# Performance work log

Hardware: AMD Instinct MI355X
Metric: run time of the kernel (lower is better)

## Reference

```python
import jax, jax.numpy as jnp
import numpy as np

D_MODEL = 1024
N_HEADS = 16
HEAD_DIM = D_MODEL // N_HEADS


def setup_inputs() -> dict:
    key = jax.random.key(0)
    ks = jax.random.split(key, 5)
    T, B = 2048, 2
    x = jax.random.normal(ks[0], (T, B, D_MODEL), dtype=jnp.float32)
    s = 1.0 / np.sqrt(D_MODEL)
    Wq = jax.random.normal(ks[1], (D_MODEL, D_MODEL), dtype=jnp.float32) * s
    Wk = jax.random.normal(ks[2], (D_MODEL, D_MODEL), dtype=jnp.float32) * s
    Wv = jax.random.normal(ks[3], (D_MODEL, D_MODEL), dtype=jnp.float32) * s
    Wo = jax.random.normal(ks[4], (D_MODEL, D_MODEL), dtype=jnp.float32) * s
    return {"x": x, "Wq": Wq, "Wk": Wk, "Wv": Wv, "Wo": Wo}


def reference(x, Wq, Wk, Wv, Wo):
    T, B, C = x.shape
    H, D = N_HEADS, HEAD_DIM

    def split_heads(t):
        # (T,B,C) -> (B,H,T,D), matching view+permute(1,2,0,3)
        return t.reshape(T, B, H, D).transpose(1, 2, 0, 3)

    q = split_heads(x @ Wq.T)
    k = split_heads(x @ Wk.T)
    v = split_heads(x @ Wv.T)

    scale = 1.0 / jnp.sqrt(jnp.asarray(D, dtype=x.dtype))
    scores = jnp.einsum('bhqd,bhkd->bhqk', q, k) * scale  # (B,H,T,T)
    causal = jnp.tril(jnp.ones((T, T), dtype=bool))
    scores = jnp.where(causal, scores, jnp.asarray(-jnp.inf, dtype=scores.dtype))
    probs = jax.nn.softmax(scores, axis=-1)
    ctx = jnp.einsum('bhqk,bhkd->bhqd', probs, v)  # (B,H,T,D)
    ctx = ctx.transpose(2, 0, 1, 3).reshape(T, B, C)
    return ctx @ Wo.T
```

## Files before the change

kernel.cpp:

```cpp
#include <hip/hip_runtime.h>
#include <hip/hip_bf16.h>

#define TT 2048
#define BB 2
#define CC 1024
#define HH 16
#define DD 64
#define MM (TT * BB)

typedef short bf16x8 __attribute__((ext_vector_type(8)));
typedef float f32x4  __attribute__((ext_vector_type(4)));

__device__ inline ushort f2b(float f) {
    union { float f; unsigned u; } v; v.f = f;
    unsigned r = v.u + 0x7FFFu + ((v.u >> 16) & 1u);
    return (ushort)(r >> 16);
}

__device__ inline unsigned pack_bf16(float a, float b) {
    __hip_bfloat162 h = __float22bfloat162_rn(make_float2(a, b));
    union { __hip_bfloat162 h; unsigned u; } c; c.h = h;
    return c.u;
}

__device__ inline void gload_lds16(const ushort* g, ushort* l) {
    __builtin_amdgcn_global_load_lds(
        (const __attribute__((address_space(1))) void*)g,
        (__attribute__((address_space(3))) void*)l, 16, 0, 0);
}

__global__ __launch_bounds__(256) void conv_x(const float* __restrict__ src,
                                              ushort* __restrict__ dst) {
    int i = blockIdx.x * 256 + threadIdx.x;
    float4 v = ((const float4*)src)[i];
    ushort4 o = {f2b(v.x), f2b(v.y), f2b(v.z), f2b(v.w)};
    ((ushort4*)dst)[i] = o;
}

__global__ __launch_bounds__(256) void conv_w(const float* __restrict__ Wq,
                                              const float* __restrict__ Wk,
                                              const float* __restrict__ Wv,
                                              const float* __restrict__ Wo,
                                              ushort* __restrict__ dst) {
    const float* s = (blockIdx.y == 0) ? Wq : (blockIdx.y == 1) ? Wk
                   : (blockIdx.y == 2) ? Wv : Wo;
    int i = blockIdx.x * 256 + threadIdx.x;
    float4 v = ((const float4*)s)[i];
    ushort4 o = {f2b(v.x), f2b(v.y), f2b(v.z), f2b(v.w)};
    ((ushort4*)(dst + (size_t)blockIdx.y * CC * CC))[i] = o;
}

template <int MODE>
__global__ __launch_bounds__(256) void gemm_mfma(const ushort* __restrict__ A,
                                                 const ushort* __restrict__ B0,
                                                 const ushort* __restrict__ B1,
                                                 const ushort* __restrict__ B2,
                                                 ushort* __restrict__ Oq,
                                                 ushort* __restrict__ Ok,
                                                 ushort* __restrict__ Ov,
                                                 float* __restrict__ Of) {
    __shared__ __align__(16) ushort As[128 * 32];
    __shared__ __align__(16) ushort Bs[128 * 32];

    const int tid = threadIdx.x;
    const int wave = tid >> 6, lane = tid & 63;
    const int quad = lane >> 4, l16 = lane & 15;
    const int wm = wave >> 1, wn = wave & 1;

    const int bm = blockIdx.x * 128;
    const ushort* Bp;
    int bn, wsel = 0;
    if (MODE == 1) {
        int by = blockIdx.y;
        wsel = by >> 3;
        Bp = (wsel == 0) ? B0 : (wsel == 1) ? B1 : B2;
        bn = (by & 7) * 128;
    } else {
        Bp = B0;
        bn = blockIdx.y * 128;
    }

    const int srow = lane >> 2;
    const int scol = (lane & 3) * 8;

    f32x4 acc[4][4];
#pragma unroll
    for (int i = 0; i < 4; i++)
#pragma unroll
        for (int j = 0; j < 4; j++) acc[i][j] = (f32x4){0.f, 0.f, 0.f, 0.f};

    for (int k0 = 0; k0 < CC; k0 += 32) {
#pragma unroll
        for (int i = 0; i < 2; i++) {
            const int rbase = wave * 32 + i * 16;
            gload_lds16(A + (size_t)(bm + rbase + srow) * CC + k0 + scol,
                        As + rbase * 32);
            gload_lds16(Bp + (size_t)(bn + rbase + srow) * CC + k0 + scol,
                        Bs + rbase * 32);
        }
        __syncthreads();

        bf16x8 af[4], bf[4];
#pragma unroll
        for (int mi = 0; mi < 4; mi++)
            af[mi] = *(const bf16x8*)(As + (wm * 64 + mi * 16 + l16) * 32 + quad * 8);
#pragma unroll
        for (int ni = 0; ni < 4; ni++)
            bf[ni] = *(const bf16x8*)(Bs + (wn * 64 + ni * 16 + l16) * 32 + quad * 8);
#pragma unroll
        for (int mi = 0; mi < 4; mi++)
#pragma unroll
            for (int ni = 0; ni < 4; ni++)
                acc[mi][ni] = __builtin_amdgcn_mfma_f32_16x16x32_bf16(
                    af[mi], bf[ni], acc[mi][ni], 0, 0, 0);
        __syncthreads();
    }

#pragma unroll
    for (int mi = 0; mi < 4; mi++) {
#pragma unroll
        for (int r = 0; r < 4; r++) {
            const int m = bm + wm * 64 + mi * 16 + quad * 4 + r;
#pragma unroll
            for (int ni = 0; ni < 4; ni++) {
                const int colg = bn + wn * 64 + ni * 16 + l16;
                float v = acc[mi][ni][r];
                if (MODE == 0) {
                    Of[(size_t)m * CC + colg] = v;
                } else {
                    if (wsel == 0) v *= 0.18033688f;
                    const int t = m >> 1, b = m & 1;
                    const int h = colg >> 6, d = colg & 63;
                    ushort* dst = (wsel == 0) ? Oq : (wsel == 1) ? Ok : Ov;
                    dst[(((size_t)(b * HH + h)) * TT + t) * DD + d] = f2b(v);
                }
            }
        }
    }
}

__global__ __launch_bounds__(256) void vtrans(const ushort* __restrict__ Vb,
                                              ushort* __restrict__ Vt) {
    __shared__ __align__(16) ushort Ls[64 * 80];
    const int bh = blockIdx.y;
    const int t0 = blockIdx.x * 64;
    const int e = threadIdx.x;
    const size_t bsrc = (size_t)bh * TT * DD;
    const size_t bdst = (size_t)bh * DD * TT;

#pragma unroll
    for (int p = 0; p < 2; p++) {
        int r = p * 32 + (e >> 3);
        int oct = e & 7;
        *(uint4*)(Ls + r * 80 + oct * 8) =
            *(const uint4*)(Vb + bsrc + (size_t)(t0 + r) * DD + oct * 8);
    }
    __syncthreads();
#pragma unroll
    for (int p = 0; p < 2; p++) {
        int d = p * 32 + (e >> 3);
        int toct = e & 7;
        ushort tmp[8];
#pragma unroll
        for (int u = 0; u < 8; u++) {
            int jp = toct * 8 + u;
            int js = (jp & 3) * 16 + (jp >> 2);
            tmp[u] = Ls[js * 80 + d];
        }
        *(uint4*)(Vt + bdst + (size_t)d * TT + t0 + toct * 8) = *(uint4*)tmp;
    }
}

template <bool DIAG>
__device__ __forceinline__ void attn_step(const bf16x8* qa, f32x4* Oacc,
                                          float* lrun,
                                          const bf16x8* kf, const bf16x8* vf,
                                          ushort* Pw, int j0, int qbase,
                                          int quad, int l16) {
    f32x4 S[4];
#pragma unroll
    for (int nb = 0; nb < 4; nb++) S[nb] = (f32x4){0.f, 0.f, 0.f, 0.f};
#pragma unroll
    for (int c = 0; c < 2; c++)
#pragma unroll
        for (int nb = 0; nb < 4; nb++)
            S[nb] = __builtin_amdgcn_mfma_f32_16x16x32_bf16(qa[c], kf[c * 4 + nb],
                                                            S[nb], 0, 0, 0);

#pragma unroll
    for (int r = 0; r < 4; r++) {
        const int qg = qbase + quad * 4 + r;
        float p[4];
#pragma unroll
        for (int nb = 0; nb < 4; nb++) {
            float s = S[nb][r];
            if (DIAG) {
                if (j0 + nb * 16 + l16 > qg) s = -1e30f;
            }
            p[nb] = __builtin_amdgcn_exp2f(fminf(s, 60.f));
        }
        lrun[r] += (p[0] + p[1]) + (p[2] + p[3]);
        uint2 w;
        w.x = pack_bf16(p[0], p[1]);
        w.y = pack_bf16(p[2], p[3]);
        *(uint2*)(Pw + (quad * 4 + r) * 72 + l16 * 4) = w;
    }

#pragma unroll
    for (int c = 0; c < 2; c++) {
        bf16x8 pa = *(const bf16x8*)(Pw + l16 * 72 + c * 32 + quad * 8);
#pragma unroll
        for (int db = 0; db < 4; db++)
            Oacc[db] = __builtin_amdgcn_mfma_f32_16x16x32_bf16(pa, vf[c * 4 + db],
                                                               Oacc[db], 0, 0, 0);
    }
}

__global__ __launch_bounds__(256, 2) void attn_mfma(const ushort* __restrict__ Qb,
                                                    const ushort* __restrict__ Kb,
                                                    const ushort* __restrict__ Vt,
                                                    ushort* __restrict__ ctx) {
    __shared__ __align__(16) ushort Ks[64 * 72];
    __shared__ __align__(16) ushort Vs[64 * 72];
    __shared__ __align__(16) ushort Ps[4 * 16 * 72];

    const int tid  = threadIdx.x;
    const int wave = tid >> 6;
    const int lane = tid & 63;
    const int quad = lane >> 4;
    const int l16  = lane & 15;

    const int p  = blockIdx.x;
    const int bh = blockIdx.y;
    const int qtA = p, qtB = (TT / 64 - 1) - p;
    const int q0A = qtA * 64 + wave * 16;
    const int q0B = qtB * 64 + wave * 16;

    const size_t baseQK = (size_t)bh * TT * DD;
    const size_t baseVt = (size_t)bh * DD * TT;

    bf16x8 qaA[2], qaB[2];
    {
        const ushort* qp = Qb + baseQK + (size_t)(q0A + l16) * DD + quad * 8;
        qaA[0] = *(const bf16x8*)(qp);
        qaA[1] = *(const bf16x8*)(qp + 32);
        const ushort* qp2 = Qb + baseQK + (size_t)(q0B + l16) * DD + quad * 8;
        qaB[0] = *(const bf16x8*)(qp2);
        qaB[1] = *(const bf16x8*)(qp2 + 32);
    }

    f32x4 OA[4], OB[4];
#pragma unroll
    for (int i = 0; i < 4; i++) {
        OA[i] = (f32x4){0.f, 0.f, 0.f, 0.f};
        OB[i] = (f32x4){0.f, 0.f, 0.f, 0.f};
    }
    float lA[4] = {0.f, 0.f, 0.f, 0.f};
    float lB[4] = {0.f, 0.f, 0.f, 0.f};

    ushort* Pw = Ps + wave * 16 * 72;

    const int row0 = tid >> 3;
    const int oct  = tid & 7;

    uint4 kr0, kr1, vr0, vr1;
    kr0 = *(const uint4*)(Kb + baseQK + (size_t)row0 * DD + oct * 8);
    kr1 = *(const uint4*)(Kb + baseQK + (size_t)(row0 + 32) * DD + oct * 8);
    vr0 = *(const uint4*)(Vt + baseVt + (size_t)row0 * TT + oct * 8);
    vr1 = *(const uint4*)(Vt + baseVt + (size_t)(row0 + 32) * TT + oct * 8);

    for (int kt = 0; kt <= qtB; kt++) {
        const int j0 = kt * 64;

        *(uint4*)(Ks + row0 * 72 + oct * 8) = kr0;
        *(uint4*)(Ks + (row0 + 32) * 72 + oct * 8) = kr1;
        *(uint4*)(Vs + row0 * 72 + oct * 8) = vr0;
        *(uint4*)(Vs + (row0 + 32) * 72 + oct * 8) = vr1;
        __syncthreads();

        if (kt < qtB) {
            const int jn = j0 + 64;
            kr0 = *(const uint4*)(Kb + baseQK + (size_t)(jn + row0) * DD + oct * 8);
            kr1 = *(const uint4*)(Kb + baseQK + (size_t)(jn + row0 + 32) * DD + oct * 8);
            vr0 = *(const uint4*)(Vt + baseVt + (size_t)row0 * TT + jn + oct * 8);
            vr1 = *(const uint4*)(Vt + baseVt + (size_t)(row0 + 32) * TT + jn + oct * 8);
        }

        bf16x8 kf[8], vf[8];
#pragma unroll
        for (int c = 0; c < 2; c++)
#pragma unroll
            for (int nb = 0; nb < 4; nb++) {
                kf[c * 4 + nb] = *(const bf16x8*)(Ks + (nb * 16 + l16) * 72 + c * 32 + quad * 8);
                vf[c * 4 + nb] = *(const bf16x8*)(Vs + (nb * 16 + l16) * 72 + c * 32 + quad * 8);
            }

        if (kt == qtB)
            attn_step<true >(qaB, OB, lB, kf, vf, Pw, j0, q0B, quad, l16);
        else
            attn_step<false>(qaB, OB, lB, kf, vf, Pw, j0, q0B, quad, l16);

        if (kt <= qtA) {
            if (kt == qtA)
                attn_step<true >(qaA, OA, lA, kf, vf, Pw, j0, q0A, quad, l16);
            else
                attn_step<false>(qaA, OA, lA, kf, vf, Pw, j0, q0A, quad, l16);
        }
        __syncthreads();
    }

    const int b = bh >> 4, h = bh & 15;
#pragma unroll
    for (int r = 0; r < 4; r++) {
        float la = lA[r], lb = lB[r];
        la += __shfl_xor(la, 1); la += __shfl_xor(la, 2);
        la += __shfl_xor(la, 4); la += __shfl_xor(la, 8);
        lb += __shfl_xor(lb, 1); lb += __shfl_xor(lb, 2);
        lb += __shfl_xor(lb, 4); lb += __shfl_xor(lb, 8);
        const float invA = 1.f / la;
        const float invB = 1.f / lb;
        const int tA = q0A + quad * 4 + r;
        const int tB = q0B + quad * 4 + r;
#pragma unroll
        for (int db = 0; db < 4; db++) {
            ctx[((size_t)tA * BB + b) * CC + h * DD + db * 16 + l16] =
                f2b(OA[db][r] * invA);
            ctx[((size_t)tB * BB + b) * CC + h * DD + db * 16 + l16] =
                f2b(OB[db][r] * invB);
        }
    }
}

extern "C" void kernel_launch(void* const* d_in, const int* in_sizes, int n_in,
                              void* d_out, int out_size, void* d_ws, size_t ws_size,
                              hipStream_t stream) {
    const float* x  = (const float*)d_in[0];
    const float* Wq = (const float*)d_in[1];
    const float* Wk = (const float*)d_in[2];
    const float* Wv = (const float*)d_in[3];
    const float* Wo = (const float*)d_in[4];
    float* out = (float*)d_out;

    ushort* xb  = (ushort*)d_ws;
    ushort* Wb  = xb + (size_t)MM * CC;
    ushort* Wqb = Wb;
    ushort* Wkb = Wb + (size_t)CC * CC;
    ushort* Wvb = Wb + 2 * (size_t)CC * CC;
    ushort* Wob = Wb + 3 * (size_t)CC * CC;
    ushort* Qb  = Wb + 4 * (size_t)CC * CC;
    ushort* Kb  = Qb + (size_t)MM * CC;
    ushort* Vb  = Kb + (size_t)MM * CC;
    ushort* Vt  = Vb + (size_t)MM * CC;
    ushort* Ctxb = Vt + (size_t)MM * CC;

    conv_x<<<dim3(MM * CC / 4 / 256), 256, 0, stream>>>(x, xb);
    conv_w<<<dim3(CC * CC / 4 / 256, 4), 256, 0, stream>>>(Wq, Wk, Wv, Wo, Wb);

    gemm_mfma<1><<<dim3(MM / 128, 24), 256, 0, stream>>>(
        xb, Wqb, Wkb, Wvb, Qb, Kb, Vb, nullptr);

    vtrans<<<dim3(TT / 64, BB * HH), 256, 0, stream>>>(Vb, Vt);

    attn_mfma<<<dim3(TT / 128, BB * HH), 256, 0, stream>>>(Qb, Kb, Vt, Ctxb);

    gemm_mfma<0><<<dim3(MM / 128, CC / 128), 256, 0, stream>>>(
        Ctxb, Wob, nullptr, nullptr, nullptr, nullptr, nullptr, out);
}
```

Baseline: 187.1 us.

## Merge conversion kernels, retile output GEMM, interleave two query tiles in attention

Replaces the separate x and weight bf16 conversion kernels with a single launch that covers all five tensors. The output projection gets its own kernel with 128x64 tiles, which doubles the block count (512 vs 256) for better CU occupancy. The attention step now processes both query tiles in one pass, sharing each K/V LDS fragment load between the two MFMA streams and using separate P buffers so the two tiles' work can interleave. The cost is more live accumulators and more LDS per block, which may lower occupancy.

After: 182.2 us. -2.6%, faster.

```diff
diff --git a/kernel.cpp b/kernel.cpp
--- a/kernel.cpp
+++ b/kernel.cpp
@@ -29,36 +29,36 @@
         (__attribute__((address_space(3))) void*)l, 16, 0, 0);
 }
 
-__global__ __launch_bounds__(256) void conv_x(const float* __restrict__ src,
-                                              ushort* __restrict__ dst) {
-    int i = blockIdx.x * 256 + threadIdx.x;
-    float4 v = ((const float4*)src)[i];
+#define XQUADS (MM * CC / 4)
+#define WQUADS (CC * CC / 4)
+__global__ __launch_bounds__(256) void conv_all(const float* __restrict__ x,
+                                                const float* __restrict__ Wq,
+                                                const float* __restrict__ Wk,
+                                                const float* __restrict__ Wv,
+                                                const float* __restrict__ Wo,
+                                                ushort* __restrict__ dst) {
+    int idx = blockIdx.x * 256 + threadIdx.x;
+    const float* src;
+    int off;
+    if (idx < XQUADS) {
+        src = x; off = idx;
+    } else {
+        int wi = (idx - XQUADS) >> 18;
+        off = (idx - XQUADS) & (WQUADS - 1);
+        src = (wi == 0) ? Wq : (wi == 1) ? Wk : (wi == 2) ? Wv : Wo;
+    }
+    float4 v = ((const float4*)src)[off];
     ushort4 o = {f2b(v.x), f2b(v.y), f2b(v.z), f2b(v.w)};
-    ((ushort4*)dst)[i] = o;
-}
-
-__global__ __launch_bounds__(256) void conv_w(const float* __restrict__ Wq,
-                                              const float* __restrict__ Wk,
-                                              const float* __restrict__ Wv,
-                                              const float* __restrict__ Wo,
-                                              ushort* __restrict__ dst) {
-    const float* s = (blockIdx.y == 0) ? Wq : (blockIdx.y == 1) ? Wk
-                   : (blockIdx.y == 2) ? Wv : Wo;
-    int i = blockIdx.x * 256 + threadIdx.x;
-    float4 v = ((const float4*)s)[i];
-    ushort4 o = {f2b(v.x), f2b(v.y), f2b(v.z), f2b(v.w)};
-    ((ushort4*)(dst + (size_t)blockIdx.y * CC * CC))[i] = o;
-}
-
-template <int MODE>
-__global__ __launch_bounds__(256) void gemm_mfma(const ushort* __restrict__ A,
-                                                 const ushort* __restrict__ B0,
-                                                 const ushort* __restrict__ B1,
-                                                 const ushort* __restrict__ B2,
-                                                 ushort* __restrict__ Oq,
-                                                 ushort* __restrict__ Ok,
-                                                 ushort* __restrict__ Ov,
-                                                 float* __restrict__ Of) {
+    ((ushort4*)dst)[idx] = o;
+}
+
+__global__ __launch_bounds__(256) void gemm_qkv(const ushort* __restrict__ A,
+                                                const ushort* __restrict__ B0,
+                                                const ushort* __restrict__ B1,
+                                                const ushort* __restrict__ B2,
+                                                ushort* __restrict__ Oq,
+                                                ushort* __restrict__ Ok,
+                                                ushort* __restrict__ Ov) {
     __shared__ __align__(16) ushort As[128 * 32];
     __shared__ __align__(16) ushort Bs[128 * 32];
 
@@ -68,17 +68,10 @@
     const int wm = wave >> 1, wn = wave & 1;
 
     const int bm = blockIdx.x * 128;
-    const ushort* Bp;
-    int bn, wsel = 0;
-    if (MODE == 1) {
-        int by = blockIdx.y;
-        wsel = by >> 3;
-        Bp = (wsel == 0) ? B0 : (wsel == 1) ? B1 : B2;
-        bn = (by & 7) * 128;
-    } else {
-        Bp = B0;
-        bn = blockIdx.y * 128;
-    }
+    const int by = blockIdx.y;
+    const int wsel = by >> 3;
+    const ushort* Bp = (wsel == 0) ? B0 : (wsel == 1) ? B1 : B2;
+    const int bn = (by & 7) * 128;
 
     const int srow = lane >> 2;
     const int scol = (lane & 3) * 8;
@@ -125,18 +118,74 @@
             for (int ni = 0; ni < 4; ni++) {
                 const int colg = bn + wn * 64 + ni * 16 + l16;
                 float v = acc[mi][ni][r];
-                if (MODE == 0) {
-                    Of[(size_t)m * CC + colg] = v;
-                } else {
-                    if (wsel == 0) v *= 0.18033688f;
-                    const int t = m >> 1, b = m & 1;
-                    const int h = colg >> 6, d = colg & 63;
-                    ushort* dst = (wsel == 0) ? Oq : (wsel == 1) ? Ok : Ov;
-                    dst[(((size_t)(b * HH + h)) * TT + t) * DD + d] = f2b(v);
-                }
+                if (wsel == 0) v *= 0.18033688f;
+                const int t = m >> 1, b = m & 1;
+                const int h = colg >> 6, d = colg & 63;
+                ushort* dst = (wsel == 0) ? Oq : (wsel == 1) ? Ok : Ov;
+                dst[(((size_t)(b * HH + h)) * TT + t) * DD + d] = f2b(v);
             }
         }
     }
+}
+
+__global__ __launch_bounds__(256) void gemm_out(const ushort* __restrict__ A,
+                                                const ushort* __restrict__ Bm,
+                                                float* __restrict__ Of) {
+    __shared__ __align__(16) ushort As[128 * 32];
+    __shared__ __align__(16) ushort Bs[64 * 32];
+
+    const int tid = threadIdx.x;
+    const int wave = tid >> 6, lane = tid & 63;
+    const int quad = lane >> 4, l16 = lane & 15;
+
+    const int bm = blockIdx.x * 128;
+    const int bn = blockIdx.y * 64;
+
+    const int srow = lane >> 2;
+    const int scol = (lane & 3) * 8;
+
+    f32x4 acc[2][4];
+#pragma unroll
+    for (int i = 0; i < 2; i++)
+#pragma unroll
+        for (int j = 0; j < 4; j++) acc[i][j] = (f32x4){0.f, 0.f, 0.f, 0.f};
+
+    for (int k0 = 0; k0 < CC; k0 += 32) {
+#pragma unroll
+        for (int i = 0; i < 2; i++) {
+            const int rbase = wave * 32 + i * 16;
+            gload_lds16(A + (size_t)(bm + rbase + srow) * CC + k0 + scol,
+                        As + rbase * 32);
+        }
+        gload_lds16(Bm + (size_t)(bn + wave * 16 + srow) * CC + k0 + scol,
+                    Bs + wave * 16 * 32);
+        __syncthreads();
+
+        bf16x8 af[2], bf[4];
+#pragma unroll
+        for (int mi = 0; mi < 2; mi++)
+            af[mi] = *(const bf16x8*)(As + (wave * 32 + mi * 16 + l16) * 32 + quad * 8);
+#pragma unroll
+        for (int ni = 0; ni < 4; ni++)
+            bf[ni] = *(const bf16x8*)(Bs + (ni * 16 + l16) * 32 + quad * 8);
+#pragma unroll
+        for (int mi = 0; mi < 2; mi++)
+#pragma unroll
+            for (int ni = 0; ni < 4; ni++)
+                acc[mi][ni] = __builtin_amdgcn_mfma_f32_16x16x32_bf16(
+                    af[mi], bf[ni], acc[mi][ni], 0, 0, 0);
+        __syncthreads();
+    }
+
+#pragma unroll
+    for (int mi = 0; mi < 2; mi++)
+#pragma unroll
+        for (int r = 0; r < 4; r++) {
+            const int m = bm + wave * 32 + mi * 16 + quad * 4 + r;
+#pragma unroll
+            for (int ni = 0; ni < 4; ni++)
+                Of[(size_t)m * CC + bn + ni * 16 + l16] = acc[mi][ni][r];
+        }
 }
 
 __global__ __launch_bounds__(256) void vtrans(const ushort* __restrict__ Vb,
@@ -171,48 +220,72 @@
     }
 }
 
-template <bool DIAG>
-__device__ __forceinline__ void attn_step(const bf16x8* qa, f32x4* Oacc,
-                                          float* lrun,
-                                          const bf16x8* kf, const bf16x8* vf,
-                                          ushort* Pw, int j0, int qbase,
-                                          int quad, int l16) {
-    f32x4 S[4];
-#pragma unroll
-    for (int nb = 0; nb < 4; nb++) S[nb] = (f32x4){0.f, 0.f, 0.f, 0.f};
+template <int AM, bool BD>
+__device__ __forceinline__ void attn_step2(const bf16x8* qaA, const bf16x8* qaB,
+                                           f32x4* OA, f32x4* OB,
+                                           float* lA, float* lB,
+                                           const ushort* Ks, const ushort* Vs,
+                                           ushort* PA, ushort* PB,
+                                           int j0, int q0A, int q0B,
+                                           int quad, int l16) {
+    f32x4 SA[4], SB[4];
+#pragma unroll
+    for (int nb = 0; nb < 4; nb++) {
+        SB[nb] = (f32x4){0.f, 0.f, 0.f, 0.f};
+        if (AM < 2) SA[nb] = (f32x4){0.f, 0.f, 0.f, 0.f};
+    }
 #pragma unroll
     for (int c = 0; c < 2; c++)
 #pragma unroll
-        for (int nb = 0; nb < 4; nb++)
-            S[nb] = __builtin_amdgcn_mfma_f32_16x16x32_bf16(qa[c], kf[c * 4 + nb],
-                                                            S[nb], 0, 0, 0);
+        for (int nb = 0; nb < 4; nb++) {
+            bf16x8 k = *(const bf16x8*)(Ks + (nb * 16 + l16) * 72 + c * 32 + quad * 8);
+            SB[nb] = __builtin_amdgcn_mfma_f32_16x16x32_bf16(qaB[c], k, SB[nb], 0, 0, 0);
+            if (AM < 2)
+                SA[nb] = __builtin_amdgcn_mfma_f32_16x16x32_bf16(qaA[c], k, SA[nb], 0, 0, 0);
+        }
 
 #pragma unroll
     for (int r = 0; r < 4; r++) {
-        const int qg = qbase + quad * 4 + r;
-        float p[4];
-#pragma unroll
-        for (int nb = 0; nb < 4; nb++) {
-            float s = S[nb][r];
-            if (DIAG) {
-                if (j0 + nb * 16 + l16 > qg) s = -1e30f;
+        {
+            const int qg = q0B + quad * 4 + r;
+            float p[4];
+#pragma unroll
+            for (int nb = 0; nb < 4; nb++) {
+                float s = SB[nb][r];
+                if (BD) { if (j0 + nb * 16 + l16 > qg) s = -1e30f; }
+                p[nb] = __builtin_amdgcn_exp2f(fminf(s, 60.f));
             }
-            p[nb] = __builtin_amdgcn_exp2f(fminf(s, 60.f));
-        }
-        lrun[r] += (p[0] + p[1]) + (p[2] + p[3]);
-        uint2 w;
-        w.x = pack_bf16(p[0], p[1]);
-        w.y = pack_bf16(p[2], p[3]);
-        *(uint2*)(Pw + (quad * 4 + r) * 72 + l16 * 4) = w;
+            lB[r] += (p[0] + p[1]) + (p[2] + p[3]);
+            uint2 w; w.x = pack_bf16(p[0], p[1]); w.y = pack_bf16(p[2], p[3]);
+            *(uint2*)(PB + (quad * 4 + r) * 72 + l16 * 4) = w;
+        }
+        if (AM < 2) {
+            const int qg = q0A + quad * 4 + r;
+            float p[4];
+#pragma unroll
+            for (int nb = 0; nb < 4; nb++) {
+                float s = SA[nb][r];
+                if (AM == 1) { if (j0 + nb * 16 + l16 > qg) s = -1e30f; }
+                p[nb] = __builtin_amdgcn_exp2f(fminf(s, 60.f));
+            }
+            lA[r] += (p[0] + p[1]) + (p[2] + p[3]);
+            uint2 w; w.x = pack_bf16(p[0], p[1]); w.y = pack_bf16(p[2], p[3]);
+            *(uint2*)(PA + (quad * 4 + r) * 72 + l16 * 4) = w;
+        }
     }
 
 #pragma unroll
     for (int c = 0; c < 2; c++) {
-        bf16x8 pa = *(const bf16x8*)(Pw + l16 * 72 + c * 32 + quad * 8);
-#pragma unroll
-        for (int db = 0; db < 4; db++)
-            Oacc[db] = __builtin_amdgcn_mfma_f32_16x16x32_bf16(pa, vf[c * 4 + db],
-                                                               Oacc[db], 0, 0, 0);
+        bf16x8 paB = *(const bf16x8*)(PB + l16 * 72 + c * 32 + quad * 8);
+        bf16x8 paA;
+        if (AM < 2) paA = *(const bf16x8*)(PA + l16 * 72 + c * 32 + quad * 8);
+#pragma unroll
+        for (int db = 0; db < 4; db++) {
+            bf16x8 v = *(const bf16x8*)(Vs + (db * 16 + l16) * 72 + c * 32 + quad * 8);
+            OB[db] = __builtin_amdgcn_mfma_f32_16x16x32_bf16(paB, v, OB[db], 0, 0, 0);
+            if (AM < 2)
+                OA[db] = __builtin_amdgcn_mfma_f32_16x16x32_bf16(paA, v, OA[db], 0, 0, 0);
+        }
     }
 }
 
@@ -222,7 +295,8 @@
                                                     ushort* __restrict__ ctx) {
     __shared__ __align__(16) ushort Ks[64 * 72];
     __shared__ __align__(16) ushort Vs[64 * 72];
-    __shared__ __align__(16) ushort Ps[4 * 16 * 72];
+    __shared__ __align__(16) ushort PsA[4 * 16 * 72];
+    __shared__ __align__(16) ushort PsB[4 * 16 * 72];
 
     const int tid  = threadIdx.x;
     const int wave = tid >> 6;
@@ -258,7 +332,8 @@
     float lA[4] = {0.f, 0.f, 0.f, 0.f};
     float lB[4] = {0.f, 0.f, 0.f, 0.f};
 
-    ushort* Pw = Ps + wave * 16 * 72;
+    ushort* PA = PsA + wave * 16 * 72;
+    ushort* PB = PsB + wave * 16 * 72;
 
     const int row0 = tid >> 3;
     const int oct  = tid & 7;
@@ -286,26 +361,18 @@
             vr1 = *(const uint4*)(Vt + baseVt + (size_t)(row0 + 32) * TT + jn + oct * 8);
         }
 
-        bf16x8 kf[8], vf[8];
-#pragma unroll
-        for (int c = 0; c < 2; c++)
-#pragma unroll
-            for (int nb = 0; nb < 4; nb++) {
-                kf[c * 4 + nb] = *(const bf16x8*)(Ks + (nb * 16 + l16) * 72 + c * 32 + quad * 8);
-                vf[c * 4 + nb] = *(const bf16x8*)(Vs + (nb * 16 + l16) * 72 + c * 32 + quad * 8);
-            }
-
-        if (kt == qtB)
-            attn_step<true >(qaB, OB, lB, kf, vf, Pw, j0, q0B, quad, l16);
+        if (kt < qtA)
+            attn_step2<0, false>(qaA, qaB, OA, OB, lA, lB, Ks, Vs, PA, PB,
+                                 j0, q0A, q0B, quad, l16);
+        else if (kt == qtA)
+            attn_step2<1, false>(qaA, qaB, OA, OB, lA, lB, Ks, Vs, PA, PB,
+                                 j0, q0A, q0B, quad, l16);
+        else if (kt < qtB)
+            attn_step2<2, false>(qaA, qaB, OA, OB, lA, lB, Ks, Vs, PA, PB,
+                                 j0, q0A, q0B, quad, l16);
         else
-            attn_step<false>(qaB, OB, lB, kf, vf, Pw, j0, q0B, quad, l16);
-
-        if (kt <= qtA) {
-            if (kt == qtA)
-                attn_step<true >(qaA, OA, lA, kf, vf, Pw, j0, q0A, quad, l16);
-            else
-                attn_step<false>(qaA, OA, lA, kf, vf, Pw, j0, q0A, quad, l16);
-        }
+            attn_step2<2, true>(qaA, qaB, OA, OB, lA, lB, Ks, Vs, PA, PB,
+                                j0, q0A, q0B, quad, l16);
         __syncthreads();
     }
 
@@ -353,16 +420,15 @@
     ushort* Vt  = Vb + (size_t)MM * CC;
     ushort* Ctxb = Vt + (size_t)MM * CC;
 
-    conv_x<<<dim3(MM * CC / 4 / 256), 256, 0, stream>>>(x, xb);
-    conv_w<<<dim3(CC * CC / 4 / 256, 4), 256, 0, stream>>>(Wq, Wk, Wv, Wo, Wb);
-
-    gemm_mfma<1><<<dim3(MM / 128, 24), 256, 0, stream>>>(
-        xb, Wqb, Wkb, Wvb, Qb, Kb, Vb, nullptr);
+    conv_all<<<dim3((XQUADS + 4 * WQUADS) / 256), 256, 0, stream>>>(
+        x, Wq, Wk, Wv, Wo, xb);
+
+    gemm_qkv<<<dim3(MM / 128, 24), 256, 0, stream>>>(
+        xb, Wqb, Wkb, Wvb, Qb, Kb, Vb);
 
     vtrans<<<dim3(TT / 64, BB * HH), 256, 0, stream>>>(Vb, Vt);
 
     attn_mfma<<<dim3(TT / 128, BB * HH), 256, 0, stream>>>(Qb, Kb, Vt, Ctxb);
 
-    gemm_mfma<0><<<dim3(MM / 128, CC / 128), 256, 0, stream>>>(
-        Ctxb, Wob, nullptr, nullptr, nullptr, nullptr, nullptr, out);
-}
+    gemm_out<<<dim3(MM / 128, CC / 64), 256, 0, stream>>>(Ctxb, Wob, out);
+}
```
